# Performance work log

Hardware: AMD Instinct MI355X
Metric: run time of the kernel (lower is better)

The kernel has to match this reference:

```python
import jax, jax.numpy as jnp
import numpy as np

B, N, IN_C, HEAD_C, H, EXPAND, OUT_C = 4, 2048, 256, 32, 8, 1024, 256
QKV_DIM = HEAD_C * H * 2 + IN_C * H  # 2560
LN_EPS = 1e-5


def setup_inputs() -> dict:
    key = jax.random.key(0)
    ks = jax.random.split(key, 6)
    s = lambda fan: 1.0 / np.sqrt(fan)
    return {
        "x": jax.random.normal(ks[0], (B, N, IN_C), jnp.float32),
        "ln1_g": jnp.ones((IN_C,), jnp.float32),
        "ln1_b": jnp.zeros((IN_C,), jnp.float32),
        "Wqkv": jax.random.normal(ks[1], (IN_C, QKV_DIM), jnp.float32) * s(IN_C),
        "bqkv": jnp.zeros((QKV_DIM,), jnp.float32),
        "Wm": jax.random.normal(ks[2], (IN_C * H, IN_C), jnp.float32) * s(IN_C * H),
        "bm": jnp.zeros((IN_C,), jnp.float32),
        "ln2_g": jnp.ones((IN_C,), jnp.float32),
        "ln2_b": jnp.zeros((IN_C,), jnp.float32),
        "W1": jax.random.normal(ks[3], (IN_C, EXPAND), jnp.float32) * s(IN_C),
        "b1": jnp.zeros((EXPAND,), jnp.float32),
        "W2": jax.random.normal(ks[4], (EXPAND, OUT_C), jnp.float32) * s(EXPAND),
        "b2": jnp.zeros((OUT_C,), jnp.float32),
    }


def _ln(x, g, b):
    m = x.mean(-1, keepdims=True)
    v = jnp.mean(jnp.square(x - m), axis=-1, keepdims=True)
    return (x - m) * jax.lax.rsqrt(v + LN_EPS) * g + b


def reference(x, ln1_g, ln1_b, Wqkv, bqkv, Wm, bm, ln2_g, ln2_b, W1, b1, W2, b2):
    scale = HEAD_C ** -0.5
    qkv = _ln(x, ln1_g, ln1_b) @ Wqkv + bqkv  # [B,N,QKV_DIM]
    q, k, v = jnp.split(qkv, [HEAD_C * H, 2 * HEAD_C * H], axis=-1)
    q = q.reshape(B, N, H, HEAD_C)  # H-major channel split, matches einops
    k = k.reshape(B, N, H, HEAD_C)
    v = v.reshape(B, N, H, IN_C)    # NOTE: V has in_c channels per head
    attn = jax.nn.softmax(jnp.einsum('bnhc,bmhc->bhnm', q, k) * scale, axis=-1)
    out = jnp.einsum('bhnm,bmhc->bnhc', attn, v).reshape(B, N, H * IN_C)
    x = x + out @ Wm + bm  # residual + merge-head projection
    h = jax.nn.gelu(_ln(x, ln2_g, ln2_b) @ W1 + b1, approximate=False)
    return (h @ W2 + b2) + x  # shortcut is Identity (in_c == out_c)
```

## Files before the change

### kernel.cpp

```cpp
#include <hip/hip_runtime.h>
#include <hip/hip_bf16.h>

typedef unsigned short u16;
typedef __attribute__((ext_vector_type(8))) short bf8_t;
typedef __attribute__((ext_vector_type(4))) float f4_t;
typedef __attribute__((ext_vector_type(16))) float fx16;

__device__ __forceinline__ float bf2f(u16 v) {
    union { unsigned u; float f; } c; c.u = ((unsigned)v) << 16; return c.f;
}
__device__ __forceinline__ u16 f2bf(float f) {
    union { float f; unsigned u; } c; c.f = f;
    unsigned r = 0x7FFFu + ((c.u >> 16) & 1u);
    return (u16)((c.u + r) >> 16);
}
__device__ __forceinline__ u16 f2bf_hw(float f) {
    union { __hip_bfloat16 b; u16 u; } c; c.b = __float2bfloat16(f); return c.u;
}

typedef __attribute__((address_space(3))) unsigned as3_u32;
typedef __attribute__((address_space(1))) const unsigned as1_u32;
__device__ __forceinline__ void gl16(const u16* g, u16* l) {
    __builtin_amdgcn_global_load_lds((as1_u32*)(const void*)g, (as3_u32*)(void*)l, 16, 0, 0);
}

#define B_   4
#define N_   2048
#define INC  256
#define H_   8
#define ROWS 8192

#define SEG_X     0
#define SEG_LN1G  2097152
#define SEG_LN1B  2097408
#define SEG_WQKV  2097664
#define SEG_BQKV  2753024
#define SEG_WM    2755584
#define SEG_BM    3279872
#define SEG_LN2G  3280128
#define SEG_LN2B  3280384
#define SEG_W1    3280640
#define SEG_B1    3542784
#define SEG_W2    3543808
#define SEG_B2    3805952
#define SEG_TOT   3806208

__device__ __forceinline__ int sniff_flag(const void* x0, int t, int* sh) {
    if (t == 0) *sh = 0;
    __syncthreads();
    int bad = 0;
    #pragma unroll
    for (int k2 = 0; k2 < 4; ++k2) {
        float v = bf2f(((const u16*)x0)[t * 4 + k2]);
        if (!(fabsf(v) < 1e10f)) bad = 1;
    }
    if (bad) atomicOr(sh, 1);
    __syncthreads();
    return *sh;
}

__global__ __launch_bounds__(256) void prep_k(
    const void* p0, const void* p1, const void* p2, const void* p3, const void* p4,
    const void* p5, const void* p6, const void* p7, const void* p8, const void* p9,
    const void* p10, const void* p11, const void* p12,
    u16* __restrict__ dst, u16* __restrict__ y, int* __restrict__ mkz)
{
    const int t = threadIdx.x;
    const int blk = blockIdx.x;
    __shared__ int sflag;
    const int flag = sniff_flag(p0, t, &sflag);

    if (blk < 8192) {
        const int i = blk * 256 + t;
        float v = flag ? ((const float*)p0)[i] : bf2f(((const u16*)p0)[i]);
        dst[i] = f2bf_hw(v);
        float s = v, s2 = v * v;
        #pragma unroll
        for (int d = 1; d < 64; d <<= 1) {
            s  += __shfl_xor(s,  d, 64);
            s2 += __shfl_xor(s2, d, 64);
        }
        __shared__ float rs[8];
        int w = t >> 6;
        if ((t & 63) == 0) { rs[w] = s; rs[4 + w] = s2; }
        __syncthreads();
        s  = rs[0] + rs[1] + rs[2] + rs[3];
        s2 = rs[4] + rs[5] + rs[6] + rs[7];
        float mean = s * (1.0f / INC);
        float var  = s2 * (1.0f / INC) - mean * mean;
        float inv  = rsqrtf(var + 1e-5f);
        float g  = flag ? ((const float*)p1)[t] : bf2f(((const u16*)p1)[t]);
        float bb = flag ? ((const float*)p2)[t] : bf2f(((const u16*)p2)[t]);
        y[i] = f2bf_hw((v - mean) * inv * g + bb);
        return;
    }

    if (blk < 8210) {
        if (blk == 8192 && t < 32) mkz[t] = 0;
        const int elem = (blk - 8192) * 256 + t;
        const void* p; int j; size_t doff;
        if      (elem < 2560) { p = p4;  j = elem;        doff = SEG_BQKV + j; }
        else if (elem < 2816) { p = p6;  j = elem - 2560; doff = SEG_BM   + j; }
        else if (elem < 3072) { p = p7;  j = elem - 2816; doff = SEG_LN2G + j; }
        else if (elem < 3328) { p = p8;  j = elem - 3072; doff = SEG_LN2B + j; }
        else if (elem < 4352) { p = p10; j = elem - 3328; doff = SEG_B1   + j; }
        else                  { p = p12; j = elem - 4352; doff = SEG_B2   + j; }
        dst[doff] = flag ? f2bf(((const float*)p)[j]) : ((const u16*)p)[j];
        return;
    }

    const int blk2 = blk - 8210;
    const void* W; int Kd, Nd, kt, nt; size_t seg;
    if (blk2 < 160)      { W = p3;  Kd = 256;  Nd = 2560; kt = blk2 / 40;  nt = blk2 % 40;  seg = SEG_WQKV; }
    else if (blk2 < 288) { int i2 = blk2 - 160; W = p5;  Kd = 2048; Nd = 256;  kt = i2 >> 2;  nt = i2 & 3;  seg = SEG_WM; }
    else if (blk2 < 352) { int i2 = blk2 - 288; W = p9;  Kd = 256;  Nd = 1024; kt = i2 >> 4;  nt = i2 & 15; seg = SEG_W1; }
    else                 { int i2 = blk2 - 352; W = p11; Kd = 1024; Nd = 256;  kt = i2 >> 2;  nt = i2 & 3;  seg = SEG_W2; }
    const int k0 = kt * 64, n0 = nt * 64;

    __shared__ u16 Tl[64][66];
    #pragma unroll
    for (int p = 0; p < 16; ++p) {
        int idx = t + p * 256;
        int r = idx >> 6, c = idx & 63;
        size_t si = (size_t)(k0 + r) * Nd + n0 + c;
        Tl[r][c] = flag ? f2bf(((const float*)W)[si]) : ((const u16*)W)[si];
    }
    __syncthreads();
    u16* dp = dst + seg;
    #pragma unroll
    for (int p = 0; p < 8; ++p) {
        int idx = t + p * 256;
        int rn = idx >> 5, ck = (idx & 31) * 2;
        ushort2 v; v.x = Tl[ck][rn]; v.y = Tl[ck + 1][rn];
        *(ushort2*)(dp + (size_t)(n0 + rn) * Kd + k0 + ck) = v;
    }
}

template<bool BF16IN>
__global__ __launch_bounds__(256) void ln_k(const void* __restrict__ xp,
        const u16* __restrict__ g, const u16* __restrict__ b, u16* __restrict__ y)
{
    int row  = blockIdx.x * 4 + (threadIdx.x >> 6);
    int lane = threadIdx.x & 63;
    int c0   = lane * 4;
    float v[4];
    if (BF16IN) {
        ushort4 u = *(const ushort4*)((const u16*)xp + (size_t)row * INC + c0);
        v[0] = bf2f(u.x); v[1] = bf2f(u.y); v[2] = bf2f(u.z); v[3] = bf2f(u.w);
    } else {
        float4 f = *(const float4*)((const float*)xp + (size_t)row * INC + c0);
        v[0] = f.x; v[1] = f.y; v[2] = f.z; v[3] = f.w;
    }
    float s = v[0] + v[1] + v[2] + v[3];
    float s2 = v[0]*v[0] + v[1]*v[1] + v[2]*v[2] + v[3]*v[3];
    #pragma unroll
    for (int d = 1; d < 64; d <<= 1) {
        s  += __shfl_xor(s,  d, 64);
        s2 += __shfl_xor(s2, d, 64);
    }
    float mean = s * (1.0f / INC);
    float var  = s2 * (1.0f / INC) - mean * mean;
    float inv  = rsqrtf(var + 1e-5f);
    ushort4 gv = *(const ushort4*)(g + c0);
    ushort4 bv = *(const ushort4*)(b + c0);
    ushort4 o;
    o.x = f2bf_hw((v[0] - mean) * inv * bf2f(gv.x) + bf2f(bv.x));
    o.y = f2bf_hw((v[1] - mean) * inv * bf2f(gv.y) + bf2f(bv.y));
    o.z = f2bf_hw((v[2] - mean) * inv * bf2f(gv.z) + bf2f(bv.z));
    o.w = f2bf_hw((v[3] - mean) * inv * bf2f(gv.w) + bf2f(bv.w));
    *(ushort4*)(y + (size_t)row * INC + c0) = o;
}

enum { EP_QKV = 0, EP_MERGE = 1, EP_GELU = 2, EP_FFN2 = 3 };

template<int MODE>
__global__ __launch_bounds__(256) void gemm_big(
    const u16* __restrict__ A, const u16* __restrict__ Bt,
    const u16* __restrict__ bias, void* __restrict__ outp,
    u16* __restrict__ qh, u16* __restrict__ kh, u16* __restrict__ vh,
    int* __restrict__ mkz, int N, int K)
{
    const int t = threadIdx.x;
    const int w = t >> 6, lane = t & 63;
    const int l15 = lane & 15, quad = lane >> 4;
    const int col0 = blockIdx.x * 64;
    const int row0 = blockIdx.y * 256;
    const int lr = lane >> 3;
    const int sc = ((lane & 7) ^ lr) * 8;

    __shared__ __align__(16) u16 Sb[20480];
    u16* Al = Sb;
    u16* Bl = Sb + 16384;

    f4_t acc[4][4];
    #pragma unroll
    for (int mi = 0; mi < 4; ++mi)
        #pragma unroll
        for (int ni = 0; ni < 4; ++ni)
            acc[mi][ni] = (f4_t){0.f, 0.f, 0.f, 0.f};

    for (int k0 = 0; k0 < K; k0 += 64) {
        #pragma unroll
        for (int i = 0; i < 8; ++i) {
            int r = w * 64 + i * 8;
            gl16(A + (size_t)(row0 + r + lr) * K + k0 + sc, Al + r * 64);
        }
        gl16(Bt + (size_t)(col0 + w * 16 + lr) * K + k0 + sc,     Bl + (w * 16) * 64);
        gl16(Bt + (size_t)(col0 + w * 16 + 8 + lr) * K + k0 + sc, Bl + (w * 16 + 8) * 64);
        __syncthreads();
        #pragma unroll
        for (int kc = 0; kc < 2; ++kc) {
            bf8_t a[4], bb[4];
            #pragma unroll
            for (int mi = 0; mi < 4; ++mi) {
                int row = w * 64 + mi * 16 + l15;
                a[mi] = *(const bf8_t*)(Al + row * 64 + ((kc * 4 + quad) ^ (row & 7)) * 8);
            }
            #pragma unroll
            for (int ni = 0; ni < 4; ++ni) {
                int row = ni * 16 + l15;
                bb[ni] = *(const bf8_t*)(Bl + row * 64 + ((kc * 4 + quad) ^ (row & 7)) * 8);
            }
            #pragma unroll
            for (int ni = 0; ni < 4; ++ni)
                #pragma unroll
                for (int mi = 0; mi < 4; ++mi)
                    acc[mi][ni] = __builtin_amdgcn_mfma_f32_16x16x32_bf16(
                        a[mi], bb[ni], acc[mi][ni], 0, 0, 0);
        }
        __syncthreads();
    }
    const int mrow = row0 + w * 64;

    if (MODE == EP_QKV) {
        if (col0 >= 512) {
            u16 (*Ts)[268] = (u16(*)[268])Sb;
            #pragma unroll
            for (int mi = 0; mi < 4; ++mi)
                #pragma unroll
                for (int ni = 0; ni < 4; ++ni) {
                    float bz = bf2f(bias[col0 + ni * 16 + l15]);
                    #pragma unroll
                    for (int r = 0; r < 4; ++r)
                        Ts[ni * 16 + l15][w * 64 + mi * 16 + quad * 4 + r] =
                            f2bf_hw(acc[mi][ni][r] + bz);
                }
            __syncthreads();
            int vcg = col0 - 512;
            int hh  = vcg >> 8;
            int bb2 = row0 >> 11, nb = row0 & 2047;
            int bhh = bb2 * 8 + hh;
            int tok4 = t & 3, cl = (t >> 2) & 63;
            int vc = (vcg & 255) + cl;
            #pragma unroll
            for (int kb = 0; kb < 16; ++kb) {
                u16* dp = vh + (((size_t)bhh * 128 + ((nb >> 4) + kb)) * 256 + vc) * 16 + tok4 * 4;
                *(ushort4*)dp = *(const ushort4*)&Ts[cl][kb * 16 + tok4 * 4];
            }
        } else if (col0 < 256) {
            #pragma unroll
            for (int mi = 0; mi < 4; ++mi)
                #pragma unroll
                for (int r = 0; r < 4; ++r) {
                    int rg = mrow + mi * 16 + quad * 4 + r;
                    int bb2 = rg >> 11, n = rg & 2047;
                    #pragma unroll
                    for (int ni = 0; ni < 4; ++ni) {
                        int col = col0 + ni * 16 + l15;
                        float v = acc[mi][ni][r] + bf2f(bias[col]);
                        qh[(((size_t)(bb2 * 8 + (col >> 5))) * 2048 + n) * 32 + (col & 31)] = f2bf_hw(v);
                    }
                }
        } else {
            const int hA  = (col0 - 256) >> 5;
            const int bb2 = row0 >> 11;
            float mxA = 0.f, mxB = 0.f;
            #pragma unroll
            for (int mi = 0; mi < 4; ++mi)
                #pragma unroll
                for (int r = 0; r < 4; ++r) {
                    int rg = mrow + mi * 16 + quad * 4 + r;
                    int n = rg & 2047;
                    float vv[4];
                    #pragma unroll
                    for (int ni = 0; ni < 4; ++ni) {
                        int col = col0 + ni * 16 + l15;
                        float v = acc[mi][ni][r] + bf2f(bias[col]);
                        vv[ni] = v;
                        int c2 = col - 256;
                        int hd = c2 >> 5, ch = c2 & 31;
                        kh[(((size_t)(bb2 * 8 + hd) * 64 + (n >> 5)) * 2 + (ch >> 4)) * 512
                           + (n & 31) * 16 + (ch & 15)] = f2bf_hw(v);
                    }
                    float sA = vv[0] * vv[0] + vv[1] * vv[1];
                    float sB = vv[2] * vv[2] + vv[3] * vv[3];
                    #pragma unroll
                    for (int d = 1; d < 16; d <<= 1) {
                        sA += __shfl_xor(sA, d, 64);
                        sB += __shfl_xor(sB, d, 64);
                    }
                    mxA = fmaxf(mxA, sA);
                    mxB = fmaxf(mxB, sB);
                }
            if ((lane & 15) == 0) {
                atomicMax(mkz + bb2 * 8 + hA,     __float_as_int(mxA));
                atomicMax(mkz + bb2 * 8 + hA + 1, __float_as_int(mxB));
            }
        }
    } else {
        u16 (*Ts2)[72] = (u16(*)[72])Sb;
        float bz[4];
        #pragma unroll
        for (int ni = 0; ni < 4; ++ni) bz[ni] = bf2f(bias[col0 + ni * 16 + l15]);
        #pragma unroll
        for (int mi = 0; mi < 4; ++mi)
            #pragma unroll
            for (int ni = 0; ni < 4; ++ni)
                #pragma unroll
                for (int r = 0; r < 4; ++r) {
                    float v = acc[mi][ni][r] + bz[ni];
                    v = 0.5f * v * (1.0f + erff(v * 0.70710678118654752f));
                    Ts2[w * 64 + mi * 16 + quad * 4 + r][ni * 16 + l15] = f2bf_hw(v);
                }
        __syncthreads();
        const int rl0 = t >> 3, c8 = (t & 7) * 8;
        #pragma unroll
        for (int p = 0; p < 8; ++p) {
            int rl = rl0 + p * 32;
            *(bf8_t*)((u16*)outp + (size_t)(row0 + rl) * N + col0 + c8) =
                *(const bf8_t*)&Ts2[rl][c8];
        }
    }
}

template<int MODE>
__global__ __launch_bounds__(256) void gemm_mfma(
    const u16* __restrict__ A, const u16* __restrict__ Bt,
    const u16* __restrict__ bias, const void* __restrict__ res,
    void* __restrict__ outp, int N, int K)
{
    const int t = threadIdx.x;
    const int w = t >> 6, lane = t & 63;
    const int l15 = lane & 15, quad = lane >> 4;
    const int col0 = blockIdx.x * 64;
    const int row0 = blockIdx.y * 128;
    const int lr = lane >> 3;
    const int sc = ((lane & 7) ^ lr) * 8;

    __shared__ __align__(16) float SBf[8704];
    u16* Al = (u16*)SBf;
    u16* Bl = (u16*)SBf + 8192;
    float (*Tf)[68] = (float(*)[68])SBf;

    f4_t acc[2][4];
    #pragma unroll
    for (int mi = 0; mi < 2; ++mi)
        #pragma unroll
        for (int ni = 0; ni < 4; ++ni)
            acc[mi][ni] = (f4_t){0.f, 0.f, 0.f, 0.f};

    for (int k0 = 0; k0 < K; k0 += 64) {
        #pragma unroll
        for (int i = 0; i < 4; ++i) {
            int r = w * 32 + i * 8;
            gl16(A + (size_t)(row0 + r + lr) * K + k0 + sc, Al + r * 64);
        }
        gl16(Bt + (size_t)(col0 + w * 16 + lr) * K + k0 + sc,     Bl + (w * 16) * 64);
        gl16(Bt + (size_t)(col0 + w * 16 + 8 + lr) * K + k0 + sc, Bl + (w * 16 + 8) * 64);
        __syncthreads();
        #pragma unroll
        for (int kc = 0; kc < 2; ++kc) {
            bf8_t a[2], bb[4];
            #pragma unroll
            for (int mi = 0; mi < 2; ++mi) {
                int row = w * 32 + mi * 16 + l15;
                a[mi] = *(const bf8_t*)(Al + row * 64 + ((kc * 4 + quad) ^ (row & 7)) * 8);
            }
            #pragma unroll
            for (int ni = 0; ni < 4; ++ni) {
                int row = ni * 16 + l15;
                bb[ni] = *(const bf8_t*)(Bl + row * 64 + ((kc * 4 + quad) ^ (row & 7)) * 8);
            }
            #pragma unroll
            for (int ni = 0; ni < 4; ++ni)
                #pragma unroll
                for (int mi = 0; mi < 2; ++mi)
                    acc[mi][ni] = __builtin_amdgcn_mfma_f32_16x16x32_bf16(
                        a[mi], bb[ni], acc[mi][ni], 0, 0, 0);
        }
        __syncthreads();
    }

    float bz[4];
    #pragma unroll
    for (int ni = 0; ni < 4; ++ni) bz[ni] = bf2f(bias[col0 + ni * 16 + l15]);
    #pragma unroll
    for (int mi = 0; mi < 2; ++mi)
        #pragma unroll
        for (int ni = 0; ni < 4; ++ni)
            #pragma unroll
            for (int r = 0; r < 4; ++r)
                Tf[w * 32 + mi * 16 + quad * 4 + r][ni * 16 + l15] = acc[mi][ni][r] + bz[ni];
    __syncthreads();

    const int rl0 = t >> 4, c4 = (t & 15) * 4;
    #pragma unroll
    for (int p = 0; p < 8; ++p) {
        int rl = rl0 + p * 16;
        float4 v = *(const float4*)&Tf[rl][c4];
        size_t base = (size_t)(row0 + rl) * N + col0 + c4;
        if (MODE == EP_MERGE) {
            ushort4 rv = *(const ushort4*)((const u16*)res + base);
            v.x += bf2f(rv.x); v.y += bf2f(rv.y); v.z += bf2f(rv.z); v.w += bf2f(rv.w);
        } else {
            float4 rv = *(const float4*)((const float*)res + base);
            v.x += rv.x; v.y += rv.y; v.z += rv.z; v.w += rv.w;
        }
        *(float4*)((float*)outp + base) = v;
    }
}

__global__ __launch_bounds__(256) void attn_k(
    const u16* __restrict__ qh, const u16* __restrict__ kh,
    const u16* __restrict__ vhT, const float* __restrict__ mk2,
    u16* __restrict__ ao)
{
    const int t = threadIdx.x;
    const int w = t >> 6, lane = t & 63;
    const int l31 = lane & 31, hi = lane >> 5;
    const int id = blockIdx.x;
    const int qt = (id >> 3) & 31;
    const int bh = (id >> 8) * 8 + (id & 7);
    const int b  = bh >> 3, h = bh & 7;
    const int n0 = qt * 64;
    const float SCALE = 0.17677669529663687f;
    const int sw = (l31 & 7) << 4;

    __shared__ __align__(16) u16 Pb[2][64][128];
    __shared__ float lds_l[4][64];
    __shared__ float lds_t[64];

    bf8_t qf[2][2];
    #pragma unroll
    for (int m = 0; m < 2; ++m)
        #pragma unroll
        for (int ks = 0; ks < 2; ++ks)
            qf[m][ks] = *(const bf8_t*)(qh + ((size_t)bh * 2048 + n0 + m * 32 + l31) * 32
                                        + ks * 16 + hi * 8);

    float mrow[2];
    #pragma unroll
    for (int m = 0; m < 2; ++m) {
        float q2 = 0.f;
        #pragma unroll
        for (int ks = 0; ks < 2; ++ks)
            #pragma unroll
            for (int i = 0; i < 8; ++i) {
                float qv = bf2f((u16)qf[m][ks][i]); q2 += qv * qv;
            }
        q2 += __shfl_xor(q2, 32, 64);
        mrow[m] = SCALE * sqrtf(q2 * mk2[bh]);
    }

    fx16 acc[2][2];
    #pragma unroll
    for (int a1 = 0; a1 < 2; ++a1)
        #pragma unroll
        for (int a2 = 0; a2 < 2; ++a2)
            #pragma unroll
            for (int e = 0; e < 16; ++e) acc[a1][a2][e] = 0.f;
    float lsum[2] = {0.f, 0.f};

    fx16 z16;
    #pragma unroll
    for (int e = 0; e < 16; ++e) z16[e] = 0.f;

    auto finish = [&](const fx16& s, int m, int g, char* base) {
        float p0 = __expf(fmaf(s[4 * g + 0], SCALE, -mrow[m]));
        float p1 = __expf(fmaf(s[4 * g + 1], SCALE, -mrow[m]));
        float p2 = __expf(fmaf(s[4 * g + 2], SCALE, -mrow[m]));
        float p3 = __expf(fmaf(s[4 * g + 3], SCALE, -mrow[m]));
        lsum[m] += (p0 + p1) + (p2 + p3);
        ushort4 pk;
        pk.x = f2bf_hw(p0); pk.y = f2bf_hw(p1); pk.z = f2bf_hw(p2); pk.w = f2bf_hw(p3);
        *(ushort4*)(base + (m * 32 + l31) * 256 + ((w * 64 + 16 * g + 8 * hi) ^ sw)) = pk;
    };

    bf8_t kA0, kA1;
    auto ldK = [&](int c) {
        const u16* kp = kh + ((size_t)bh * 64 + c * 4 + w) * 1024 + l31 * 16 + hi * 8;
        kA0 = *(const bf8_t*)kp;
        kA1 = *(const bf8_t*)(kp + 512);
    };

    {
        ldK(0);
        fx16 sA = __builtin_amdgcn_mfma_f32_32x32x16_bf16(kA0, qf[0][0], z16, 0, 0, 0);
        sA = __builtin_amdgcn_mfma_f32_32x32x16_bf16(kA1, qf[0][1], sA, 0, 0, 0);
        fx16 sB = __builtin_amdgcn_mfma_f32_32x32x16_bf16(kA0, qf[1][0], z16, 0, 0, 0);
        sB = __builtin_amdgcn_mfma_f32_32x32x16_bf16(kA1, qf[1][1], sB, 0, 0, 0);
        ldK(1);
        char* base0 = (char*)&Pb[0][0][0];
        #pragma unroll
        for (int g = 0; g < 4; ++g) finish(sA, 0, g, base0);
        #pragma unroll
        for (int g = 0; g < 4; ++g) finish(sB, 1, g, base0);
    }

    const u16* vpb = vhT + (((size_t)bh * 128) * 256 + w * 64 + l31) * 16 + hi * 8;
    bf8_t vb0 = *(const bf8_t*)vpb;
    bf8_t vb1 = *(const bf8_t*)(vpb + 512);

    int buf = 0;
    for (int c = 0; c < 16; ++c, buf ^= 1) {
        __syncthreads();
        const bool qn = (c < 15);
        fx16 sA, sB;
        if (qn) {
            sA = __builtin_amdgcn_mfma_f32_32x32x16_bf16(kA0, qf[0][0], z16, 0, 0, 0);
            sA = __builtin_amdgcn_mfma_f32_32x32x16_bf16(kA1, qf[0][1], sA, 0, 0, 0);
        }
        const char* pb = (const char*)&Pb[buf][0][0];
        char* wr = (char*)&Pb[buf ^ 1][0][0];
        const u16* vp = vpb + (size_t)c * 32768;
        #pragma unroll
        for (int ks = 0; ks < 8; ++ks) {
            bf8_t nv0 = *(const bf8_t*)(vp + (ks + 1) * 4096);
            bf8_t nv1 = *(const bf8_t*)(vp + (ks + 1) * 4096 + 512);
            bf8_t pa0 = *(const bf8_t*)(pb + l31 * 256        + ((ks * 32 + hi * 16) ^ sw));
            bf8_t pa1 = *(const bf8_t*)(pb + (32 + l31) * 256 + ((ks * 32 + hi * 16) ^ sw));
            __builtin_amdgcn_s_setprio(1);
            acc[0][0] = __builtin_amdgcn_mfma_f32_32x32x16_bf16(pa0, vb0, acc[0][0], 0, 0, 0);
            acc[0][1] = __builtin_amdgcn_mfma_f32_32x32x16_bf16(pa0, vb1, acc[0][1], 0, 0, 0);
            acc[1][0] = __builtin_amdgcn_mfma_f32_32x32x16_bf16(pa1, vb0, acc[1][0], 0, 0, 0);
            acc[1][1] = __builtin_amdgcn_mfma_f32_32x32x16_bf16(pa1, vb1, acc[1][1], 0, 0, 0);
            __builtin_amdgcn_s_setprio(0);
            if (qn) {
                if (ks < 4) {
                    finish(sA, 0, ks, wr);
                    if (ks == 3) {
                        sB = __builtin_amdgcn_mfma_f32_32x32x16_bf16(kA0, qf[1][0], z16, 0, 0, 0);
                        sB = __builtin_amdgcn_mfma_f32_32x32x16_bf16(kA1, qf[1][1], sB, 0, 0, 0);
                        if (c < 14) ldK(c + 2);
                    }
                } else {
                    finish(sB, 1, ks - 4, wr);
                }
            }
            vb0 = nv0; vb1 = nv1;
        }
    }

    #pragma unroll
    for (int m = 0; m < 2; ++m) {
        lsum[m] += __shfl_xor(lsum[m], 32, 64);
        if (hi == 0) lds_l[w][m * 32 + l31] = lsum[m];
    }
    __syncthreads();
    if (t < 64) lds_t[t] = lds_l[0][t] + lds_l[1][t] + lds_l[2][t] + lds_l[3][t];
    __syncthreads();

    #pragma unroll
    for (int mt = 0; mt < 2; ++mt)
        #pragma unroll
        for (int g = 0; g < 4; ++g) {
            f4_t lv = *(const f4_t*)&lds_t[mt * 32 + 8 * g + 4 * hi];
            #pragma unroll
            for (int j = 0; j < 4; ++j) {
                float inv = 1.0f / lv[j];
                int q = mt * 32 + 8 * g + 4 * hi + j;
                size_t rowbase = ((size_t)(b * 2048 + n0 + q)) * 2048 + h * 256 + w * 64;
                #pragma unroll
                for (int nt = 0; nt < 2; ++nt)
                    ao[rowbase + nt * 32 + l31] = f2bf_hw(acc[mt][nt][g * 4 + j] * inv);
            }
        }
}

extern "C" void kernel_launch(void* const* d_in, const int* in_sizes, int n_in,
                              void* d_out, int out_size, void* d_ws, size_t ws_size,
                              hipStream_t stream)
{
    u16* wsu = (u16*)d_ws;
    float* mk = (float*)(wsu + 64);

    const size_t CVT0 = 128;
    const size_t Y0   = CVT0 + SEG_TOT;
    const size_t QH0  = Y0  + 2097152;
    const size_t KH0  = QH0 + 2097152;
    const size_t VT0  = KH0 + 2097152;
    const size_t AO0  = VT0 + 16777216;
    const size_t X20  = AO0 + 16777216;

    u16* cvt = wsu + CVT0;
    u16* y   = wsu + Y0;
    u16* qh  = wsu + QH0;
    u16* kh  = wsu + KH0;
    u16* vhT = wsu + VT0;
    u16* ao  = wsu + AO0;
    float* x2 = (float*)(wsu + X20);
    u16* hbb  = wsu + AO0;

    const u16* xc   = cvt + SEG_X;
    const u16* Wqkv = cvt + SEG_WQKV;
    const u16* bqkv = cvt + SEG_BQKV;
    const u16* Wm   = cvt + SEG_WM;
    const u16* bm   = cvt + SEG_BM;
    const u16* ln2g = cvt + SEG_LN2G;
    const u16* ln2b = cvt + SEG_LN2B;
    const u16* W1   = cvt + SEG_W1;
    const u16* b1   = cvt + SEG_B1;
    const u16* W2   = cvt + SEG_W2;
    const u16* b2   = cvt + SEG_B2;

    prep_k<<<8626, 256, 0, stream>>>(
        d_in[0], d_in[1], d_in[2], d_in[3], d_in[4], d_in[5], d_in[6],
        d_in[7], d_in[8], d_in[9], d_in[10], d_in[11], d_in[12],
        cvt, y, (int*)mk);

    gemm_big<EP_QKV><<<dim3(2560 / 64, ROWS / 256), 256, 0, stream>>>(
        y, Wqkv, bqkv, nullptr, qh, kh, vhT, (int*)mk, 2560, 256);
    attn_k<<<1024, 256, 0, stream>>>(qh, kh, vhT, mk, ao);
    gemm_mfma<EP_MERGE><<<dim3(256 / 64, ROWS / 128), 256, 0, stream>>>(
        ao, Wm, bm, xc, x2, 256, 2048);
    ln_k<false><<<ROWS / 4, 256, 0, stream>>>(x2, ln2g, ln2b, y);
    gemm_big<EP_GELU><<<dim3(1024 / 64, ROWS / 256), 256, 0, stream>>>(
        y, W1, b1, hbb, nullptr, nullptr, nullptr, nullptr, 1024, 256);
    gemm_mfma<EP_FFN2><<<dim3(256 / 64, ROWS / 128), 256, 0, stream>>>(
        hbb, W2, b2, x2, d_out, 256, 1024);
}
```

Before: 294.8 us.

## Double-buffer LDS tiles in both MFMA GEMM kernels to overlap loads with compute

Both GEMM kernels now keep two LDS tile buffers. The async global-to-LDS loads for the next K-tile are issued right after the barrier, before the MFMA work on the current tile, and one barrier per iteration is dropped. The aim is to hide global load latency behind matrix math. In exchange, per-block LDS roughly doubles for the big GEMM and grows for the smaller one, which can cut how many blocks fit on each CU.

```diff
diff --git a/kernel.cpp b/kernel.cpp
--- a/kernel.cpp
+++ b/kernel.cpp
@@ -188,18 +188,11 @@
     const int lr = lane >> 3;
     const int sc = ((lane & 7) ^ lr) * 8;
 
-    __shared__ __align__(16) u16 Sb[20480];
-    u16* Al = Sb;
-    u16* Bl = Sb + 16384;
-
-    f4_t acc[4][4];
-    #pragma unroll
-    for (int mi = 0; mi < 4; ++mi)
-        #pragma unroll
-        for (int ni = 0; ni < 4; ++ni)
-            acc[mi][ni] = (f4_t){0.f, 0.f, 0.f, 0.f};
-
-    for (int k0 = 0; k0 < K; k0 += 64) {
+    __shared__ __align__(16) u16 Sb[40960];
+
+    auto stage = [&](int cur, int k0) {
+        u16* Al = Sb + cur * 20480;
+        u16* Bl = Al + 16384;
         #pragma unroll
         for (int i = 0; i < 8; ++i) {
             int r = w * 64 + i * 8;
@@ -207,7 +200,23 @@
         }
         gl16(Bt + (size_t)(col0 + w * 16 + lr) * K + k0 + sc,     Bl + (w * 16) * 64);
         gl16(Bt + (size_t)(col0 + w * 16 + 8 + lr) * K + k0 + sc, Bl + (w * 16 + 8) * 64);
+    };
+
+    f4_t acc[4][4];
+    #pragma unroll
+    for (int mi = 0; mi < 4; ++mi)
+        #pragma unroll
+        for (int ni = 0; ni < 4; ++ni)
+            acc[mi][ni] = (f4_t){0.f, 0.f, 0.f, 0.f};
+
+    const int nt = K >> 6;
+    int cur = 0;
+    stage(0, 0);
+    for (int t2 = 0; t2 < nt; ++t2, cur ^= 1) {
         __syncthreads();
+        if (t2 + 1 < nt) stage(cur ^ 1, (t2 + 1) << 6);
+        const u16* Al = Sb + cur * 20480;
+        const u16* Bl = Al + 16384;
         #pragma unroll
         for (int kc = 0; kc < 2; ++kc) {
             bf8_t a[4], bb[4];
@@ -228,8 +237,8 @@
                     acc[mi][ni] = __builtin_amdgcn_mfma_f32_16x16x32_bf16(
                         a[mi], bb[ni], acc[mi][ni], 0, 0, 0);
         }
-        __syncthreads();
-    }
+    }
+    __syncthreads();
     const int mrow = row0 + w * 64;
 
     if (MODE == EP_QKV) {
@@ -347,19 +356,12 @@
     const int lr = lane >> 3;
     const int sc = ((lane & 7) ^ lr) * 8;
 
-    __shared__ __align__(16) float SBf[8704];
-    u16* Al = (u16*)SBf;
-    u16* Bl = (u16*)SBf + 8192;
-    float (*Tf)[68] = (float(*)[68])SBf;
-
-    f4_t acc[2][4];
-    #pragma unroll
-    for (int mi = 0; mi < 2; ++mi)
-        #pragma unroll
-        for (int ni = 0; ni < 4; ++ni)
-            acc[mi][ni] = (f4_t){0.f, 0.f, 0.f, 0.f};
-
-    for (int k0 = 0; k0 < K; k0 += 64) {
+    __shared__ __align__(16) u16 Sm[24576];
+    float (*Tf)[68] = (float(*)[68])Sm;
+
+    auto stage = [&](int cur, int k0) {
+        u16* Al = Sm + cur * 12288;
+        u16* Bl = Al + 8192;
         #pragma unroll
         for (int i = 0; i < 4; ++i) {
             int r = w * 32 + i * 8;
@@ -367,7 +369,23 @@
         }
         gl16(Bt + (size_t)(col0 + w * 16 + lr) * K + k0 + sc,     Bl + (w * 16) * 64);
         gl16(Bt + (size_t)(col0 + w * 16 + 8 + lr) * K + k0 + sc, Bl + (w * 16 + 8) * 64);
+    };
+
+    f4_t acc[2][4];
+    #pragma unroll
+    for (int mi = 0; mi < 2; ++mi)
+        #pragma unroll
+        for (int ni = 0; ni < 4; ++ni)
+            acc[mi][ni] = (f4_t){0.f, 0.f, 0.f, 0.f};
+
+    const int nt = K >> 6;
+    int cur = 0;
+    stage(0, 0);
+    for (int t2 = 0; t2 < nt; ++t2, cur ^= 1) {
         __syncthreads();
+        if (t2 + 1 < nt) stage(cur ^ 1, (t2 + 1) << 6);
+        const u16* Al = Sm + cur * 12288;
+        const u16* Bl = Al + 8192;
         #pragma unroll
         for (int kc = 0; kc < 2; ++kc) {
             bf8_t a[2], bb[4];
@@ -388,8 +406,8 @@
                     acc[mi][ni] = __builtin_amdgcn_mfma_f32_16x16x32_bf16(
                         a[mi], bb[ni], acc[mi][ni], 0, 0, 0);
         }
-        __syncthreads();
-    }
+    }
+    __syncthreads();
 
     float bz[4];
     #pragma unroll
@@ -571,8 +589,8 @@
                 int q = mt * 32 + 8 * g + 4 * hi + j;
                 size_t rowbase = ((size_t)(b * 2048 + n0 + q)) * 2048 + h * 256 + w * 64;
                 #pragma unroll
-                for (int nt = 0; nt < 2; ++nt)
-                    ao[rowbase + nt * 32 + l31] = f2bf_hw(acc[mt][nt][g * 4 + j] * inv);
+                for (int nt2 = 0; nt2 < 2; ++nt2)
+                    ao[rowbase + nt2 * 32 + l31] = f2bf_hw(acc[mt][nt2][g * 4 + j] * inv);
             }
         }
 }
```

Result: faster. 273.1 us (-7.4%).
